# Optimization experiments

Measured on AMD Instinct MI355X. Metric: run time of the kernel, lower is better.

Reference implementation:

```python
import jax, jax.numpy as jnp
import numpy as np

C_S, C_P, C_H, H, P_QK, P_V = 384, 128, 16, 12, 4, 8
B, N = 1, 512
INF = 1e5
EPS = 1e-8


def quat_to_rot(q):
    w, x, y, z = q[..., 0], q[..., 1], q[..., 2], q[..., 3]
    return jnp.stack([
        jnp.stack([1 - 2 * (y * y + z * z), 2 * (x * y - w * z), 2 * (x * z + w * y)], -1),
        jnp.stack([2 * (x * y + w * z), 1 - 2 * (x * x + z * z), 2 * (y * z - w * x)], -1),
        jnp.stack([2 * (x * z - w * y), 2 * (y * z + w * x), 1 - 2 * (x * x + y * y)], -1),
    ], -2)


def layer_norm(x, g, b):
    m = x.mean(-1, keepdims=True)
    v = ((x - m) ** 2).mean(-1, keepdims=True)
    return (x - m) * jax.lax.rsqrt(v + 1e-5) * g + b


def setup_inputs():
    key = jax.random.key(0)
    ks = iter(jax.random.split(key, 64))

    def w(shape, scale=0.02):
        return jax.random.normal(next(ks), shape, dtype=jnp.float32) * scale

    inp = {}
    inp['s'] = jax.random.normal(next(ks), (B, N, C_S), dtype=jnp.float32)
    inp['p'] = jax.random.normal(next(ks), (B, N, N, C_P), dtype=jnp.float32)
    q = jax.random.normal(next(ks), (B, N, 4), dtype=jnp.float32)
    inp['rot'] = quat_to_rot(q / jnp.linalg.norm(q, axis=-1, keepdims=True))
    inp['trans'] = jax.random.normal(next(ks), (B, N, 3), dtype=jnp.float32)
    inp['mask'] = jnp.ones((B, N), dtype=jnp.float32)
    inp['w_q'] = w((C_S, H * C_H)); inp['b_q'] = jnp.zeros((H * C_H,), jnp.float32)
    inp['w_kv'] = w((C_S, 2 * H * C_H)); inp['b_kv'] = jnp.zeros((2 * H * C_H,), jnp.float32)
    inp['w_qp'] = w((C_S, H * P_QK * 3)); inp['b_qp'] = jnp.zeros((H * P_QK * 3,), jnp.float32)
    inp['w_kvp'] = w((C_S, H * (P_QK + P_V) * 3)); inp['b_kvp'] = jnp.zeros((H * (P_QK + P_V) * 3,), jnp.float32)
    inp['w_b'] = w((C_P, H)); inp['b_b'] = jnp.zeros((H,), jnp.float32)
    inp['head_w'] = w((H,), 0.5)
    d_out = H * (C_H + C_P + P_V * 4)  # 2112
    inp['w_o'] = w((d_out, C_S)); inp['b_o'] = jnp.zeros((C_S,), jnp.float32)
    inp['ln1_g'] = jnp.ones((C_S,), jnp.float32); inp['ln1_b'] = jnp.zeros((C_S,), jnp.float32)
    for i in (1, 2, 3):
        inp['tw%d' % i] = w((C_S, C_S)); inp['tb%d' % i] = jnp.zeros((C_S,), jnp.float32)
    inp['ln2_g'] = jnp.ones((C_S,), jnp.float32); inp['ln2_b'] = jnp.zeros((C_S,), jnp.float32)
    inp['bb_w'] = w((C_S, 6)); inp['bb_b'] = jnp.zeros((6,), jnp.float32)
    return inp


def forward(s, p, rot, trans, mask, w_q, b_q, w_kv, b_kv, w_qp, b_qp, w_kvp, b_kvp,
            w_b, b_b, head_w, w_o, b_o, ln1_g, ln1_b,
            tw1, tb1, tw2, tb2, tw3, tb3, ln2_g, ln2_b, bb_w, bb_b):
    # ---- Invariant Point Attention ----
    q = (s @ w_q + b_q).reshape(B, N, H, C_H)
    k, v = jnp.split((s @ w_kv + b_kv).reshape(B, N, H, 2 * C_H), 2, axis=-1)
    qp = (s @ w_qp + b_qp).reshape(B, N, H * P_QK, 3)
    qp = (jnp.einsum('bnij,bnpj->bnpi', rot, qp) + trans[:, :, None, :]).reshape(B, N, H, P_QK, 3)
    kvp = (s @ w_kvp + b_kvp).reshape(B, N, H * (P_QK + P_V), 3)
    kvp = (jnp.einsum('bnij,bnpj->bnpi', rot, kvp) + trans[:, :, None, :]).reshape(B, N, H, P_QK + P_V, 3)
    kp, vp = kvp[..., :P_QK, :], kvp[..., P_QK:, :]
    bias = p @ w_b + b_b  # [B,N,N,H]
    a = jnp.einsum('bihc,bjhc->bhij', q, k) * float(np.sqrt(1.0 / (3 * C_H)))
    a = a + float(np.sqrt(1.0 / 3)) * jnp.transpose(bias, (0, 3, 1, 2))
    d2 = ((qp[:, :, None] - kp[:, None]) ** 2).sum(-1)  # [B,N,N,H,Pqk]
    hw = jax.nn.softplus(head_w) * float(np.sqrt(1.0 / (3 * (P_QK * 9.0 / 2))))
    pt_att = -0.5 * (d2 * hw[:, None]).sum(-1)  # [B,N,N,H]
    sq_mask = (mask[:, :, None] * mask[:, None, :] - 1.0) * INF  # [B,N,N]
    a = jax.nn.softmax(a + jnp.transpose(pt_att, (0, 3, 1, 2)) + sq_mask[:, None], axis=-1)
    o = jnp.einsum('bhij,bjhc->bihc', a, v).reshape(B, N, H * C_H)
    op = jnp.einsum('bhij,bjhpc->bihpc', a, vp) - trans[:, :, None, None, :]
    op = jnp.einsum('bnji,bnhpj->bnhpi', rot, op)  # invert-apply frames
    op_norm = jnp.sqrt((op ** 2).sum(-1) + EPS)  # [B,N,H,Pv]
    o_pair = jnp.einsum('bhij,bijc->bihc', a, p).reshape(B, N, H * C_P)
    cat = jnp.concatenate([o, op.reshape(B, N, H * P_V * 3), op_norm.reshape(B, N, H * P_V), o_pair], -1)
    s = s + cat @ w_o + b_o
    s = layer_norm(s, ln1_g, ln1_b)
    # ---- structure transition (1 layer, residual + LN) ----
    h = jax.nn.relu(s @ tw1 + tb1)
    h = jax.nn.relu(h @ tw2 + tb2)
    s = layer_norm(s + h @ tw3 + tb3, ln2_g, ln2_b)
    # ---- backbone update + frame compose ----
    upd = s @ bb_w + bb_b  # [B,N,6]
    quat = jnp.concatenate([jnp.ones((B, N, 1), s.dtype), upd[..., :3]], -1)
    quat = quat / jnp.linalg.norm(quat, axis=-1, keepdims=True)
    r_u = quat_to_rot(quat)
    rot_new = jnp.einsum('bnij,bnjk->bnik', rot, r_u)
    trans_new = jnp.einsum('bnij,bnj->bni', rot, upd[..., 3:]) + trans
    return s, rot_new, trans_new


def reference(s, p, rot, trans, mask, w_q, b_q, w_kv, b_kv, w_qp, b_qp, w_kvp, b_kvp,
              w_b, b_b, head_w, w_o, b_o, ln1_g, ln1_b,
              tw1, tb1, tw2, tb2, tw3, tb3, ln2_g, ln2_b, bb_w, bb_b):
    return forward(s, p, rot, trans, mask, w_q, b_q, w_kv, b_kv, w_qp, b_qp, w_kvp, b_kvp,
                   w_b, b_b, head_w, w_o, b_o, ln1_g, ln1_b,
                   tw1, tb1, tw2, tb2, tw3, tb3, ln2_g, ln2_b, bb_w, bb_b)
```

## Files before the change

kernel.cpp:

```cpp
#include <hip/hip_runtime.h>
#include <math.h>

#define N 512
#define CS 384
#define CP 128
#define CH 16
#define NH 12
#define NN (N*N)
#define DCAT 2112
#define INFV 100000.0f

__device__ __constant__ float SC_QK = 0.14433756729740643f;
#define SC_B  0.57735026918962576f
#define HW_SC 0.13608276348795434f

typedef __attribute__((ext_vector_type(8))) short bf16x8;
typedef __attribute__((ext_vector_type(4))) float f32x4;
typedef __attribute__((ext_vector_type(4))) short sh4;
typedef __attribute__((ext_vector_type(4))) unsigned u32x4;
typedef unsigned short ushort_t;

__device__ inline short f2bf(float v) {
    unsigned u = __builtin_bit_cast(unsigned, v);
    u += 0x7FFF + ((u >> 16) & 1);
    return (short)(u >> 16);
}
__device__ inline float bf2f(ushort_t u) {
    unsigned x = ((unsigned)u) << 16;
    return __builtin_bit_cast(float, x);
}
__device__ __forceinline__ unsigned cvtpk(float a, float b) {
    unsigned r;
    asm("v_cvt_pk_bf16_f32 %0, %1, %2" : "=v"(r) : "v"(a), "v"(b));
    return r;
}

__device__ __forceinline__ void gload16(const void* g, void* l) {
    __builtin_amdgcn_global_load_lds(
        (const __attribute__((address_space(1))) unsigned int*)g,
        (__attribute__((address_space(3))) unsigned int*)l,
        16, 0, 0);
}

struct FrontArgs {
    const float* wsrc0; const float* wsrc1; const float* wsrc2; const float* wsrc3;
    const float* wsrc4; const float* wsrc5; const float* wsrc6; const float* wsrc7;
    ushort_t* wdst0; ushort_t* wdst1; ushort_t* wdst2; ushort_t* wdst3;
    ushort_t* wdst4; ushort_t* wdst5; ushort_t* wdst6; ushort_t* wdst7;
    const float* s; ushort_t* sbf;
    const float* bq; const float* bkv; const float* bqp; const float* bkvp;
    float* biasp;
    const float* p; const float* w_b; const float* b_b; ushort_t* bias_b;
};

__global__ __launch_bounds__(256) void front_kernel(FrontArgs a)
{
    __shared__ __align__(16) char SM[36864];
    const int b = blockIdx.x;
    const int t = threadIdx.x;
    if (b < 4096) {
        float* Pf = (float*)SM;
        ushort_t* Wbs = (ushort_t*)(SM + 32768);
        const int w = t >> 6;
        const size_t row0 = (size_t)b * 64;

        for (int idx = t; idx < 2048; idx += 256) {
            int h = idx >> 7, c = idx & 127;
            float v = (h < 12) ? a.w_b[c * 12 + h] : 0.f;
            int byte = h * 256 + ((c * 2) ^ ((h & 7) << 4));
            *(ushort_t*)((char*)Wbs + byte) = (ushort_t)f2bf(v);
        }
        #pragma unroll
        for (int k = 0; k < 8; ++k) {
            int s2 = k * 256 + t;
            int row = s2 >> 5, ch = s2 & 31;
            const char* src = (const char*)(a.p + (row0 + row) * 128) + ((ch ^ (row & 7)) * 16);
            gload16(src, (char*)Pf + (size_t)(k * 256 + w * 64) * 16);
        }
        __syncthreads();

        const int l = t & 63, lr = l & 15, hk = l >> 4;
        const int jb = w * 16;
        f32x4 acc = (f32x4){0.f, 0.f, 0.f, 0.f};
        #pragma unroll
        for (int ks = 0; ks < 4; ++ks) {
            int row = jb + lr;
            int kc = ks * 8 + hk * 2;
            const char* base = (const char*)Pf + row * 512;
            f32x4 v0 = *(const f32x4*)(base + ((kc ^ (row & 7)) * 16));
            f32x4 v1 = *(const f32x4*)(base + (((kc + 1) ^ (row & 7)) * 16));
            bf16x8 afr;
            afr[0] = f2bf(v0[0]); afr[1] = f2bf(v0[1]); afr[2] = f2bf(v0[2]); afr[3] = f2bf(v0[3]);
            afr[4] = f2bf(v1[0]); afr[5] = f2bf(v1[1]); afr[6] = f2bf(v1[2]); afr[7] = f2bf(v1[3]);
            bf16x8 bfr = *(const bf16x8*)((char*)Wbs + lr * 256 +
                            ((ks * 64 + hk * 16) ^ ((lr & 7) << 4)));
            acc = __builtin_amdgcn_mfma_f32_16x16x32_bf16(afr, bfr, acc, 0, 0, 0);
        }
        if (lr < 12) {
            float bb = a.b_b[lr];
            size_t gj = row0 + jb + hk * 4;
            sh4 o;
            #pragma unroll
            for (int r = 0; r < 4; ++r) o[r] = f2bf(SC_B * (acc[r] + bb));
            *(sh4*)(a.bias_b + (size_t)lr * NN + gj) = o;
        }
    } else {
        const int bp = b - 4096;
        if (bp < 1668) {
            const float* src; ushort_t* dst; int begin, nx, Nc, K;
            if      (bp < 72)   { src=a.wsrc0; dst=a.wdst0; begin=0;    nx=6;  Nc=192; K=384; }
            else if (bp < 216)  { src=a.wsrc1; dst=a.wdst1; begin=72;   nx=12; Nc=384; K=384; }
            else if (bp < 276)  { src=a.wsrc2; dst=a.wdst2; begin=216;  nx=5;  Nc=144; K=384; }
            else if (bp < 444)  { src=a.wsrc3; dst=a.wdst3; begin=276;  nx=14; Nc=432; K=384; }
            else if (bp < 1236) { src=a.wsrc4; dst=a.wdst4; begin=444;  nx=12; Nc=384; K=2112; }
            else if (bp < 1380) { src=a.wsrc5; dst=a.wdst5; begin=1236; nx=12; Nc=384; K=384; }
            else if (bp < 1524) { src=a.wsrc6; dst=a.wdst6; begin=1380; nx=12; Nc=384; K=384; }
            else                { src=a.wsrc7; dst=a.wdst7; begin=1524; nx=12; Nc=384; K=384; }
            int lb = bp - begin;
            int cx = (lb % nx) * 32, ky = (lb / nx) * 32;
            float (*tile)[33] = (float(*)[33])SM;
            const int tx = t & 31, ty = t >> 5;
            for (int r = ty; r < 32; r += 8) {
                int c = cx + tx;
                tile[r][tx] = (c < Nc) ? src[(size_t)(ky + r) * Nc + c] : 0.f;
            }
            __syncthreads();
            for (int r = ty; r < 32; r += 8) {
                int orow = cx + r;
                if (orow < Nc)
                    dst[(size_t)orow * K + ky + tx] = (ushort_t)f2bf(tile[tx][r]);
            }
        } else if (bp < 1860) {
            int i4 = (bp - 1668) * 256 + t;
            f32x4 v = *(const f32x4*)(a.s + (size_t)i4 * 4);
            sh4 o;
            o[0] = f2bf(v[0]); o[1] = f2bf(v[1]); o[2] = f2bf(v[2]); o[3] = f2bf(v[3]);
            *(sh4*)(a.sbf + (size_t)i4 * 4) = o;
        } else {
            for (int idx = t; idx < 1152; idx += 256) {
                float v;
                if (idx < 192)      v = a.bq[idx];
                else if (idx < 576) v = a.bkv[idx - 192];
                else if (idx < 720) v = a.bqp[idx - 576];
                else                v = a.bkvp[idx - 720];
                a.biasp[idx] = v;
            }
        }
    }
}

__global__ __launch_bounds__(256) void gemm_bf16(
    const ushort_t* __restrict__ A, const ushort_t* __restrict__ Bt,
    float* __restrict__ part, int K, int KOUT, int nk)
{
    __shared__ __align__(16) ushort_t As[2][2048];
    __shared__ __align__(16) ushort_t Bs[2][2048];
    const int t = threadIdx.x, w = t >> 6, l = t & 63;
    const int i0 = blockIdx.x * 64, n0 = blockIdx.y * 64, sp = blockIdx.z;
    const int kbase = sp * nk * 32;

    const int srow = w * 16 + (l >> 2);
    const int skb = (l & 3) ^ ((srow >> 1) & 3);
    const ushort_t* aSrc = A + (size_t)(i0 + srow) * K + kbase + skb * 8;
    const ushort_t* bSrc = Bt + (size_t)(n0 + srow) * K + kbase + skb * 8;
    ushort_t* aDst = &As[0][0] + w * 512;
    ushort_t* bDst = &Bs[0][0] + w * 512;

    const int r0 = (w >> 1) * 32, c0 = (w & 1) * 32, lr = l & 15, hk = l >> 4;
    int aOff[2], bOff[2];
    #pragma unroll
    for (int m = 0; m < 2; ++m) {
        int row = r0 + m * 16 + lr;
        aOff[m] = row * 64 + ((hk ^ ((row >> 1) & 3)) << 4);
    }
    #pragma unroll
    for (int n = 0; n < 2; ++n) {
        int row = c0 + n * 16 + lr;
        bOff[n] = row * 64 + ((hk ^ ((row >> 1) & 3)) << 4);
    }

    f32x4 acc[2][2];
    #pragma unroll
    for (int m = 0; m < 2; ++m)
        #pragma unroll
        for (int n = 0; n < 2; ++n) acc[m][n] = (f32x4){0.f, 0.f, 0.f, 0.f};

    gload16(aSrc, aDst);
    gload16(bSrc, bDst);
    __syncthreads();

    int cur = 0;
    for (int it = 0; it < nk; ++it) {
        if (it + 1 < nk) {
            gload16(aSrc + (it + 1) * 32, aDst + (cur ^ 1) * 2048);
            gload16(bSrc + (it + 1) * 32, bDst + (cur ^ 1) * 2048);
        }
        const char* ab = (const char*)&As[cur][0];
        const char* bb = (const char*)&Bs[cur][0];
        bf16x8 a0 = *(const bf16x8*)(ab + aOff[0]);
        bf16x8 a1 = *(const bf16x8*)(ab + aOff[1]);
        bf16x8 b0 = *(const bf16x8*)(bb + bOff[0]);
        bf16x8 b1 = *(const bf16x8*)(bb + bOff[1]);
        acc[0][0] = __builtin_amdgcn_mfma_f32_16x16x32_bf16(a0, b0, acc[0][0], 0, 0, 0);
        acc[0][1] = __builtin_amdgcn_mfma_f32_16x16x32_bf16(a0, b1, acc[0][1], 0, 0, 0);
        acc[1][0] = __builtin_amdgcn_mfma_f32_16x16x32_bf16(a1, b0, acc[1][0], 0, 0, 0);
        acc[1][1] = __builtin_amdgcn_mfma_f32_16x16x32_bf16(a1, b1, acc[1][1], 0, 0, 0);
        __syncthreads();
        cur ^= 1;
    }

    #pragma unroll
    for (int m = 0; m < 2; ++m)
        #pragma unroll
        for (int n = 0; n < 2; ++n) {
            int col = n0 + c0 + n * 16 + lr;
            int rowb = i0 + r0 + m * 16 + (l >> 4) * 4;
            float* pr = part + ((size_t)sp * 512 + rowb) * KOUT + col;
            #pragma unroll
            for (int j = 0; j < 4; ++j)
                pr[(size_t)j * KOUT] = acc[m][n][j];
        }
}

__global__ __launch_bounds__(256) void gemm_red(
    const float* __restrict__ partsIn, const float* __restrict__ kbias,
    const ushort_t* __restrict__ Bt, float* __restrict__ partOut, int nk)
{
    __shared__ __align__(16) ushort_t As[2][2048];
    __shared__ __align__(16) ushort_t Bs[2][2048];
    const int t = threadIdx.x, w = t >> 6, l = t & 63;
    const int i0 = blockIdx.x * 64, n0 = blockIdx.y * 64, sp = blockIdx.z;
    const int kbase = sp * nk * 32;

    const int srow = w * 16 + (l >> 2);
    const int skb = (l & 3) ^ ((srow >> 1) & 3);
    const ushort_t* bSrc = Bt + (size_t)(n0 + srow) * 384 + kbase + skb * 8;
    ushort_t* bDst = &Bs[0][0] + w * 512;

    const int ar = t >> 2, apch = t & 3;
    const int agch = apch ^ ((ar >> 1) & 3);
    const float* aBase = partsIn + (size_t)(i0 + ar) * 384 + kbase + agch * 8;
    const int aByte = ar * 64 + apch * 16;

    const int r0 = (w >> 1) * 32, c0 = (w & 1) * 32, lr = l & 15, hk = l >> 4;
    int aOff[2], bOff[2];
    #pragma unroll
    for (int m = 0; m < 2; ++m) {
        int row = r0 + m * 16 + lr;
        aOff[m] = row * 64 + ((hk ^ ((row >> 1) & 3)) << 4);
    }
    #pragma unroll
    for (int n = 0; n < 2; ++n) {
        int row = c0 + n * 16 + lr;
        bOff[n] = row * 64 + ((hk ^ ((row >> 1) & 3)) << 4);
    }

    f32x4 av0, av1;
    #define A_LOAD(it)                                                            \
        {                                                                         \
            const float* ap = aBase + (it) * 32;                                  \
            av0 = *(const f32x4*)(ap) + *(const f32x4*)(ap + 196608)              \
                + *(const f32x4*)(ap + 393216);                                   \
            av1 = *(const f32x4*)(ap + 4) + *(const f32x4*)(ap + 196608 + 4)      \
                + *(const f32x4*)(ap + 393216 + 4);                               \
        }
    #define A_STORE(buf, it)                                                      \
        {                                                                         \
            int kk = kbase + (it) * 32 + agch * 8;                                \
            f32x4 kb0 = *(const f32x4*)(kbias + kk);                              \
            f32x4 kb1 = *(const f32x4*)(kbias + kk + 4);                          \
            f32x4 s0 = av0 + kb0, s1 = av1 + kb1;                                 \
            u32x4 pk;                                                             \
            pk[0] = cvtpk(fmaxf(s0[0], 0.f), fmaxf(s0[1], 0.f));                  \
            pk[1] = cvtpk(fmaxf(s0[2], 0.f), fmaxf(s0[3], 0.f));                  \
            pk[2] = cvtpk(fmaxf(s1[0], 0.f), fmaxf(s1[1], 0.f));                  \
            pk[3] = cvtpk(fmaxf(s1[2], 0.f), fmaxf(s1[3], 0.f));                  \
            *(u32x4*)((char*)&As[buf][0] + aByte) = pk;                           \
        }

    f32x4 acc[2][2];
    #pragma unroll
    for (int m = 0; m < 2; ++m)
        #pragma unroll
        for (int n = 0; n < 2; ++n) acc[m][n] = (f32x4){0.f, 0.f, 0.f, 0.f};

    gload16(bSrc, bDst);
    A_LOAD(0);
    A_STORE(0, 0);
    __syncthreads();

    int cur = 0;
    for (int it = 0; it < nk; ++it) {
        if (it + 1 < nk) {
            gload16(bSrc + (it + 1) * 32, bDst + (cur ^ 1) * 2048);
            A_LOAD(it + 1);
        }
        const char* ab = (const char*)&As[cur][0];
        const char* bb = (const char*)&Bs[cur][0];
        bf16x8 a0 = *(const bf16x8*)(ab + aOff[0]);
        bf16x8 a1 = *(const bf16x8*)(ab + aOff[1]);
        bf16x8 b0 = *(const bf16x8*)(bb + bOff[0]);
        bf16x8 b1 = *(const bf16x8*)(bb + bOff[1]);
        acc[0][0] = __builtin_amdgcn_mfma_f32_16x16x32_bf16(a0, b0, acc[0][0], 0, 0, 0);
        acc[0][1] = __builtin_amdgcn_mfma_f32_16x16x32_bf16(a0, b1, acc[0][1], 0, 0, 0);
        acc[1][0] = __builtin_amdgcn_mfma_f32_16x16x32_bf16(a1, b0, acc[1][0], 0, 0, 0);
        acc[1][1] = __builtin_amdgcn_mfma_f32_16x16x32_bf16(a1, b1, acc[1][1], 0, 0, 0);
        if (it + 1 < nk) A_STORE(cur ^ 1, it + 1);
        __syncthreads();
        cur ^= 1;
    }
    #undef A_LOAD
    #undef A_STORE

    #pragma unroll
    for (int m = 0; m < 2; ++m)
        #pragma unroll
        for (int n = 0; n < 2; ++n) {
            int col = n0 + c0 + n * 16 + lr;
            int rowb = i0 + r0 + m * 16 + (l >> 4) * 4;
            float* pr = partOut + ((size_t)sp * 512 + rowb) * 384 + col;
            #pragma unroll
            for (int j = 0; j < 4; ++j)
                pr[(size_t)j * 384] = acc[m][n][j];
        }
}

__global__ void reduce_ln(const float* __restrict__ parts, int S,
                          const float* __restrict__ gbias, const float* __restrict__ resid,
                          const float* __restrict__ g, const float* __restrict__ b,
                          float* __restrict__ outf, ushort_t* __restrict__ outbf,
                          const float* __restrict__ bb_w, const float* __restrict__ bb_b,
                          const float* __restrict__ rot, const float* __restrict__ trans,
                          float* __restrict__ out_rot, float* __restrict__ out_trans)
{
    __shared__ float buf[384];
    __shared__ float red[2], red2[2];
    __shared__ float ush[2][6];
    const int i = blockIdx.x, t = threadIdx.x;
    float s = 0.f, sq = 0.f;
    for (int k = t; k < 384; k += 128) {
        float v = gbias[k] + resid[(size_t)i * 384 + k];
        for (int s2 = 0; s2 < S; ++s2)
            v += parts[((size_t)s2 * 512 + i) * 384 + k];
        buf[k] = v; s += v; sq += v * v;
    }
    for (int off = 32; off; off >>= 1) { s += __shfl_xor(s, off); sq += __shfl_xor(sq, off); }
    if ((t & 63) == 0) { red[t >> 6] = s; red2[t >> 6] = sq; }
    __syncthreads();
    float mean = (red[0] + red[1]) * (1.0f / 384.0f);
    float var = (red2[0] + red2[1]) * (1.0f / 384.0f) - mean * mean;
    float rstd = rsqrtf(var + 1e-5f);
    float onorm[3];
    #pragma unroll
    for (int kk = 0; kk < 3; ++kk) {
        int k = t + kk * 128;
        float o = (buf[k] - mean) * rstd * g[k] + b[k];
        onorm[kk] = o;
        if (outf) outf[(size_t)i * 384 + k] = o;
        if (outbf) outbf[(size_t)i * 384 + k] = (ushort_t)f2bf(o);
    }
    if (!bb_w) return;
    float u[6] = {0.f, 0.f, 0.f, 0.f, 0.f, 0.f};
    #pragma unroll
    for (int kk = 0; kk < 3; ++kk) {
        int k = t + kk * 128;
        float sv = onorm[kk];
        #pragma unroll
        for (int c = 0; c < 6; ++c) u[c] += sv * bb_w[k * 6 + c];
    }
    #pragma unroll
    for (int c = 0; c < 6; ++c)
        for (int off = 32; off; off >>= 1) u[c] += __shfl_xor(u[c], off);
    if ((t & 63) == 0) {
        #pragma unroll
        for (int c = 0; c < 6; ++c) ush[t >> 6][c] = u[c];
    }
    __syncthreads();
    if (t == 0) {
        float uu[6];
        #pragma unroll
        for (int c = 0; c < 6; ++c) uu[c] = ush[0][c] + ush[1][c] + bb_b[c];
        float inq = rsqrtf(1.0f + uu[0]*uu[0] + uu[1]*uu[1] + uu[2]*uu[2]);
        float w = inq, x = uu[0]*inq, y = uu[1]*inq, z = uu[2]*inq;
        float Ru[9];
        Ru[0] = 1.f - 2.f*(y*y + z*z); Ru[1] = 2.f*(x*y - w*z); Ru[2] = 2.f*(x*z + w*y);
        Ru[3] = 2.f*(x*y + w*z); Ru[4] = 1.f - 2.f*(x*x + z*z); Ru[5] = 2.f*(y*z - w*x);
        Ru[6] = 2.f*(x*z - w*y); Ru[7] = 2.f*(y*z + w*x); Ru[8] = 1.f - 2.f*(x*x + y*y);
        const float* R = rot + i * 9;
        #pragma unroll
        for (int a = 0; a < 3; ++a) {
            #pragma unroll
            for (int cc = 0; cc < 3; ++cc)
                out_rot[i * 9 + a * 3 + cc] =
                    R[a*3+0]*Ru[0+cc] + R[a*3+1]*Ru[3+cc] + R[a*3+2]*Ru[6+cc];
            out_trans[i * 3 + a] = R[a*3+0]*uu[3] + R[a*3+1]*uu[4] + R[a*3+2]*uu[5]
                                   + trans[i * 3 + a];
        }
    }
}

__global__ __launch_bounds__(256) void postproj_kernel(
    const float* __restrict__ parts, const float* __restrict__ biasp,
    const float* __restrict__ rot, const float* __restrict__ trans,
    const float* __restrict__ head_w, const float* __restrict__ mask,
    ushort_t* __restrict__ Qext, ushort_t* __restrict__ Kext, ushort_t* __restrict__ Vext)
{
    __shared__ float buf[1152];
    __shared__ float hwv[12], kc28[12];
    const int j = blockIdx.x, t = threadIdx.x;
    for (int c = t; c < 1152; c += 256)
        buf[c] = biasp[c] + parts[(size_t)j * 1152 + c] + parts[(size_t)(512 + j) * 1152 + c];
    if (t >= 192 && t < 204) {
        int h = t - 192;
        hwv[h] = HW_SC * log1pf(expf(head_w[h]));
    }
    __syncthreads();
    if (t < 192) {
        int base = 576 + t * 3;
        const float* R = rot + j * 9;
        const float* T = trans + j * 3;
        float x = buf[base], y = buf[base + 1], z = buf[base + 2];
        float nx = R[0]*x + R[1]*y + R[2]*z + T[0];
        float ny = R[3]*x + R[4]*y + R[5]*z + T[1];
        float nz = R[6]*x + R[7]*y + R[8]*z + T[2];
        buf[base] = nx; buf[base + 1] = ny; buf[base + 2] = nz;
    }
    __syncthreads();
    if (t < 12) {
        float s2 = 0.f;
        #pragma unroll
        for (int e = 0; e < 12; ++e) { float v = buf[720 + t * 36 + e]; s2 += v * v; }
        kc28[t] = -0.5f * hwv[t] * s2 + (mask[j] - 1.0f) * INFV;
    }
    __syncthreads();
    if (t < 192) {
        int h = t >> 4, c0 = (t & 15) * 2;
        float hwf = hwv[h];
        #pragma unroll
        for (int e = 0; e < 2; ++e) {
            int c = c0 + e;
            float qv, kv2;
            if (c < 16)      { qv = SC_QK * buf[h * 16 + c];           kv2 = buf[192 + h * 32 + c]; }
            else if (c < 28) { qv = hwf * buf[576 + h * 12 + (c - 16)]; kv2 = buf[720 + h * 36 + (c - 16)]; }
            else if (c == 28){ qv = 1.f;                               kv2 = kc28[h]; }
            else             { qv = 0.f;                               kv2 = 0.f; }
            Qext[(size_t)h * 16384 + j * 32 + c] = (ushort_t)f2bf(qv);
            Kext[(size_t)h * 16384 + j * 32 + c] = (ushort_t)f2bf(kv2);
        }
    }
    for (int idx = t; idx < 576; idx += 256) {
        int h = idx / 48, c = idx % 48;
        float v;
        if (c < 16)      v = buf[192 + h * 32 + 16 + c];
        else if (c < 40) v = buf[720 + h * 36 + 12 + (c - 16)];
        else             v = 0.f;
        Vext[(size_t)h * 24576 + c * 512 + j] = (ushort_t)f2bf(v);
    }
}

__global__ __launch_bounds__(256) void attn_mfma(
    const ushort_t* __restrict__ Qext, const ushort_t* __restrict__ Kext,
    const ushort_t* __restrict__ bias_b, const ushort_t* __restrict__ Vext,
    const float* __restrict__ rot, const float* __restrict__ trans,
    ushort_t* __restrict__ attn_b, ushort_t* __restrict__ catb)
{
    __shared__ float sc[16 * 516];
    __shared__ float redm[64];
    __shared__ float invr[16];
    __shared__ float opl[16][25];
    const int t = threadIdx.x, w = t >> 6, l = t & 63;
    const int i0 = blockIdx.x * 16, h = blockIdx.y;
    const int lr = l & 15, hk = l >> 4;

    #pragma unroll
    for (int it = 0; it < 8; ++it) {
        int elem = (t + it * 256) * 4;
        int i = elem >> 9, j = elem & 511;
        sh4 raw = *(const sh4*)(bias_b + (size_t)h * NN + (size_t)(i0 + i) * 512 + j);
        f32x4 v;
        v[0] = bf2f((ushort_t)raw[0]); v[1] = bf2f((ushort_t)raw[1]);
        v[2] = bf2f((ushort_t)raw[2]); v[3] = bf2f((ushort_t)raw[3]);
        *(f32x4*)(sc + i * 516 + j) = v;
    }
    __syncthreads();

    bf16x8 a0 = *(const bf16x8*)(Qext + (size_t)h * 16384 + (i0 + lr) * 32 + hk * 8);
    f32x4 acc[8];
    #pragma unroll
    for (int n = 0; n < 8; ++n) {
        bf16x8 b = *(const bf16x8*)(Kext + (size_t)h * 16384 +
                                    (w * 128 + n * 16 + lr) * 32 + hk * 8);
        acc[n] = __builtin_amdgcn_mfma_f32_16x16x32_bf16(a0, b, (f32x4){0.f,0.f,0.f,0.f}, 0, 0, 0);
    }

    float rmax[4] = {-3.0e38f, -3.0e38f, -3.0e38f, -3.0e38f};
    #pragma unroll
    for (int n = 0; n < 8; ++n) {
        int col = w * 128 + n * 16 + lr;
        #pragma unroll
        for (int r = 0; r < 4; ++r) {
            int row = hk * 4 + r;
            float v = acc[n][r] + sc[row * 516 + col];
            sc[row * 516 + col] = v;
            rmax[r] = fmaxf(rmax[r], v);
        }
    }
    #pragma unroll
    for (int r = 0; r < 4; ++r) {
        float v = rmax[r];
        v = fmaxf(v, __shfl_xor(v, 1));
        v = fmaxf(v, __shfl_xor(v, 2));
        v = fmaxf(v, __shfl_xor(v, 4));
        v = fmaxf(v, __shfl_xor(v, 8));
        if (lr == 0) redm[w * 16 + hk * 4 + r] = v;
    }
    __syncthreads();

    {
        int row = t >> 4, g = t & 15;
        float mx = fmaxf(fmaxf(redm[row], redm[16 + row]),
                         fmaxf(redm[32 + row], redm[48 + row]));
        float sum = 0.f;
        float* sr = sc + row * 516;
        for (int c = g; c < 512; c += 16) {
            float e = expf(sr[c] - mx);
            sr[c] = e;
            sum += e;
        }
        sum += __shfl_xor(sum, 1);
        sum += __shfl_xor(sum, 2);
        sum += __shfl_xor(sum, 4);
        sum += __shfl_xor(sum, 8);
        if (g == 0) invr[row] = 1.0f / sum;
    }
    __syncthreads();

    #pragma unroll
    for (int it = 0; it < 8; ++it) {
        int elem = (t + it * 256) * 4;
        int i = elem >> 9, j = elem & 511;
        f32x4 v = *(const f32x4*)(sc + i * 516 + j);
        float iv = invr[i];
        sh4 o;
        o[0] = f2bf(v[0] * iv); o[1] = f2bf(v[1] * iv);
        o[2] = f2bf(v[2] * iv); o[3] = f2bf(v[3] * iv);
        *(sh4*)(attn_b + (size_t)h * NN + (size_t)(i0 + i) * 512 + j) = o;
    }

    f32x4 acc3[3];
    acc3[0] = (f32x4){0.f,0.f,0.f,0.f};
    acc3[1] = (f32x4){0.f,0.f,0.f,0.f};
    acc3[2] = (f32x4){0.f,0.f,0.f,0.f};
    const ushort_t* vbase = Vext + (size_t)h * 24576 + lr * 512 + hk * 8;
    #pragma unroll
    for (int kt = 0; kt < 16; ++kt) {
        const float* srow = sc + lr * 516 + kt * 32 + hk * 8;
        f32x4 x0 = *(const f32x4*)(srow);
        f32x4 x1 = *(const f32x4*)(srow + 4);
        u32x4 ap;
        ap[0] = cvtpk(x0[0], x0[1]); ap[1] = cvtpk(x0[2], x0[3]);
        ap[2] = cvtpk(x1[0], x1[1]); ap[3] = cvtpk(x1[2], x1[3]);
        bf16x8 af = __builtin_bit_cast(bf16x8, ap);
        #pragma unroll
        for (int n = 0; n < 3; ++n) {
            bf16x8 bf = *(const bf16x8*)(vbase + n * 16 * 512 + kt * 32);
            acc3[n] = __builtin_amdgcn_mfma_f32_16x16x32_bf16(af, bf, acc3[n], 0, 0, 0);
        }
    }
    #pragma unroll
    for (int n = 0; n < 3; ++n) {
        int c = n * 16 + lr;
        #pragma unroll
        for (int r = 0; r < 4; ++r) {
            int ri = hk * 4 + r;
            float val = acc3[n][r] * invr[ri];
            if (c < 16)
                catb[(size_t)(i0 + ri) * DCAT + h * 16 + c] = (ushort_t)f2bf(val);
            else if (c < 40)
                opl[ri][c - 16] = val;
        }
    }
    __syncthreads();
    if (t < 128) {
        int i16 = t >> 3, pv = t & 7;
        int i = i0 + i16;
        const float* T = trans + i * 3;
        const float* R = rot + i * 9;
        float x = opl[i16][pv * 3 + 0] - T[0];
        float y = opl[i16][pv * 3 + 1] - T[1];
        float z = opl[i16][pv * 3 + 2] - T[2];
        float rx = R[0] * x + R[3] * y + R[6] * z;
        float ry = R[1] * x + R[4] * y + R[7] * z;
        float rz = R[2] * x + R[5] * y + R[8] * z;
        float nm = sqrtf(rx * rx + ry * ry + rz * rz + 1e-8f);
        ushort_t* cr = catb + (size_t)i * DCAT;
        cr[192 + h * 24 + pv * 3 + 0] = (ushort_t)f2bf(rx);
        cr[192 + h * 24 + pv * 3 + 1] = (ushort_t)f2bf(ry);
        cr[192 + h * 24 + pv * 3 + 2] = (ushort_t)f2bf(rz);
        cr[480 + h * 8 + pv] = (ushort_t)f2bf(nm);
    }
}

__global__ __launch_bounds__(256) void opair_mfma(
    const ushort_t* __restrict__ attn_b, const float* __restrict__ p,
    ushort_t* __restrict__ catb)
{
    __shared__ __align__(16) ushort_t As2[16 * 512];
    __shared__ __align__(16) ushort_t Pt[2][128 * 72];
    const int t = threadIdx.x, i = blockIdx.x;
    const int w = t >> 6, l = t & 63;
    const int lr = l & 15, hk = l >> 4;

    #pragma unroll
    for (int ii = 0; ii < 4; ++ii) {
        int idx = (t + ii * 256) * 8;
        int h = idx >> 9, j = idx & 511;
        bf16x8 v;
        if (h < 12) v = *(const bf16x8*)(attn_b + (size_t)h * NN + (size_t)i * 512 + j);
        else        v = (bf16x8){0,0,0,0,0,0,0,0};
        *(bf16x8*)((char*)As2 + h * 1024 + ((j * 2) ^ ((h & 7) << 4))) = v;
    }

    const int jA = (t >> 3) * 2;
    const int c0 = (t & 7) * 16;
    const float* psrc = p + (size_t)i * 65536;

    f32x4 va[4], vb[4];
    #pragma unroll
    for (int q = 0; q < 4; ++q) {
        va[q] = *(const f32x4*)(psrc + (size_t)jA * 128 + c0 + q * 4);
        vb[q] = *(const f32x4*)(psrc + (size_t)(jA + 1) * 128 + c0 + q * 4);
    }

    #define PACK_TILE(buf)                                                       \
        {                                                                        \
            ushort_t* ptw = &Pt[buf][0];                                         \
            _Pragma("unroll")                                                    \
            for (int e = 0; e < 16; ++e) {                                       \
                int c = c0 + e;                                                  \
                unsigned pk = cvtpk(va[e >> 2][e & 3], vb[e >> 2][e & 3]);       \
                int byte = c * 144 + ((jA * 2) ^ (((c >> 4) & 7) << 4));         \
                *(unsigned*)((char*)ptw + byte) = pk;                            \
            }                                                                    \
        }
    #define LOAD_TILE(tile)                                                      \
        {                                                                        \
            const float* s0 = psrc + (size_t)((tile) * 64 + jA) * 128 + c0;      \
            _Pragma("unroll")                                                    \
            for (int q = 0; q < 4; ++q) {                                        \
                va[q] = *(const f32x4*)(s0 + q * 4);                             \
                vb[q] = *(const f32x4*)(s0 + 128 + q * 4);                       \
            }                                                                    \
        }

    PACK_TILE(0);
    LOAD_TILE(1);

    f32x4 acc[2];
    acc[0] = (f32x4){0.f, 0.f, 0.f, 0.f};
    acc[1] = (f32x4){0.f, 0.f, 0.f, 0.f};

    int cur = 0;
    for (int tile = 0; tile < 8; ++tile) {
        __syncthreads();
        const char* pt = (const char*)&Pt[cur][0];
        #pragma unroll
        for (int ks = 0; ks < 2; ++ks) {
            bf16x8 afr = *(const bf16x8*)((char*)As2 + lr * 1024 +
                            ((tile * 128 + ks * 64 + hk * 16) ^ ((lr & 7) << 4)));
            #pragma unroll
            for (int n = 0; n < 2; ++n) {
                int c = w * 32 + n * 16 + lr;
                bf16x8 bfr = *(const bf16x8*)(pt + c * 144 +
                                ((ks * 64 + hk * 16) ^ (((c >> 4) & 7) << 4)));
                acc[n] = __builtin_amdgcn_mfma_f32_16x16x32_bf16(afr, bfr, acc[n], 0, 0, 0);
            }
        }
        if (tile < 7) {
            PACK_TILE(cur ^ 1);
            if (tile < 6) LOAD_TILE(tile + 2);
            cur ^= 1;
        }
    }
    #undef PACK_TILE
    #undef LOAD_TILE
    #pragma unroll
    for (int n = 0; n < 2; ++n) {
        int c = w * 32 + n * 16 + lr;
        #pragma unroll
        for (int r = 0; r < 4; ++r) {
            int h = hk * 4 + r;
            if (h < 12)
                catb[(size_t)i * DCAT + 576 + h * 128 + c] = (ushort_t)f2bf(acc[n][r]);
        }
    }
}

extern "C" void kernel_launch(void* const* d_in, const int* in_sizes, int n_in,
                              void* d_out, int out_size, void* d_ws, size_t ws_size,
                              hipStream_t stream)
{
    const float* s      = (const float*)d_in[0];
    const float* p      = (const float*)d_in[1];
    const float* rot    = (const float*)d_in[2];
    const float* trans  = (const float*)d_in[3];
    const float* mask   = (const float*)d_in[4];
    const float* w_q    = (const float*)d_in[5];
    const float* b_q    = (const float*)d_in[6];
    const float* w_kv   = (const float*)d_in[7];
    const float* b_kv   = (const float*)d_in[8];
    const float* w_qp   = (const float*)d_in[9];
    const float* b_qp   = (const float*)d_in[10];
    const float* w_kvp  = (const float*)d_in[11];
    const float* b_kvp  = (const float*)d_in[12];
    const float* w_b    = (const float*)d_in[13];
    const float* b_b    = (const float*)d_in[14];
    const float* head_w = (const float*)d_in[15];
    const float* w_o    = (const float*)d_in[16];
    const float* b_o    = (const float*)d_in[17];
    const float* ln1_g  = (const float*)d_in[18];
    const float* ln1_b  = (const float*)d_in[19];
    const float* tw1    = (const float*)d_in[20];
    const float* tb1    = (const float*)d_in[21];
    const float* tw2    = (const float*)d_in[22];
    const float* tb2    = (const float*)d_in[23];
    const float* tw3    = (const float*)d_in[24];
    const float* tb3    = (const float*)d_in[25];
    const float* ln2_g  = (const float*)d_in[26];
    const float* ln2_b  = (const float*)d_in[27];
    const float* bb_w   = (const float*)d_in[28];
    const float* bb_b   = (const float*)d_in[29];

    float* ws = (float*)d_ws;
    float*    parts  = ws;
    float*    partsB = parts + 589824;
    float*    s1     = parts + 1179648;
    float*    biasp  = s1 + 196608;
    ushort_t* ub     = (ushort_t*)(biasp + 1152);
    ushort_t* bias_b = ub;
    ushort_t* attn_b = bias_b + 3145728;
    ushort_t* catb   = attn_b + 3145728;
    ushort_t* sbf    = catb + 1081344;
    ushort_t* s1bf   = sbf + 196608;
    ushort_t* h1bf   = s1bf + 196608;
    ushort_t* h2bf   = h1bf + 196608;
    ushort_t* Qext   = h2bf + 196608;
    ushort_t* Kext   = Qext + 196608;
    ushort_t* Vext   = Kext + 196608;
    ushort_t* Wtp    = Vext + 294912;
    ushort_t* Wto    = Wtp + 442368;
    ushort_t* Wt1    = Wto + 811008;
    ushort_t* Wt2    = Wt1 + 147456;
    ushort_t* Wt3    = Wt2 + 147456;

    float* out_s     = (float*)d_out;
    float* out_rot   = out_s + 196608;
    float* out_trans = out_rot + 4608;

    FrontArgs fa;
    fa.wsrc0 = w_q;  fa.wdst0 = Wtp;
    fa.wsrc1 = w_kv; fa.wdst1 = Wtp + (size_t)192 * 384;
    fa.wsrc2 = w_qp; fa.wdst2 = Wtp + (size_t)576 * 384;
    fa.wsrc3 = w_kvp; fa.wdst3 = Wtp + (size_t)720 * 384;
    fa.wsrc4 = w_o;  fa.wdst4 = Wto;
    fa.wsrc5 = tw1;  fa.wdst5 = Wt1;
    fa.wsrc6 = tw2;  fa.wdst6 = Wt2;
    fa.wsrc7 = tw3;  fa.wdst7 = Wt3;
    fa.s = s; fa.sbf = sbf;
    fa.bq = b_q; fa.bkv = b_kv; fa.bqp = b_qp; fa.bkvp = b_kvp;
    fa.biasp = biasp;
    fa.p = p; fa.w_b = w_b; fa.b_b = b_b; fa.bias_b = bias_b;
    front_kernel<<<5957, 256, 0, stream>>>(fa);

    gemm_bf16<<<dim3(8, 18, 2), 256, 0, stream>>>(sbf, Wtp, parts, 384, 1152, 6);
    postproj_kernel<<<512, 256, 0, stream>>>(parts, biasp, rot, trans, head_w, mask,
                                             Qext, Kext, Vext);

    attn_mfma<<<dim3(32, 12), 256, 0, stream>>>(Qext, Kext, bias_b, Vext, rot, trans,
                                                attn_b, catb);
    opair_mfma<<<512, 256, 0, stream>>>(attn_b, p, catb);

    gemm_bf16<<<dim3(8, 6, 6), 256, 0, stream>>>(catb, Wto, parts, 2112, 384, 11);
    reduce_ln<<<512, 128, 0, stream>>>(parts, 6, b_o, s, ln1_g, ln1_b, s1, s1bf,
                                       nullptr, nullptr, nullptr, nullptr, nullptr, nullptr);

    gemm_bf16<<<dim3(8, 6, 3), 256, 0, stream>>>(s1bf, Wt1, parts, 384, 384, 4);
    gemm_red<<<dim3(8, 6, 3), 256, 0, stream>>>(parts, tb1, Wt2, partsB, 4);
    gemm_red<<<dim3(8, 6, 3), 256, 0, stream>>>(partsB, tb2, Wt3, parts, 4);
    reduce_ln<<<512, 128, 0, stream>>>(parts, 3, tb3, s1, ln2_g, ln2_b, out_s, nullptr,
                                       bb_w, bb_b, rot, trans, out_rot, out_trans);
}
```

Before: 124.7 us.

## Split opair reduction over j across two 256-thread groups per block

The o_pair kernel now runs 512 threads per block, and each half of the block handles 256 of the 512 j positions, using smaller 32-row p tiles with their own double-buffered LDS staging. The two partial accumulators are combined through an LDS scratch buffer before the bf16 store. The aim is more memory-level parallelism when streaming the 256 KB p slice per row, so each block finishes its load phase sooner. The cost is more LDS, an extra barrier, and a cross-group reduction, which may lower occupancy.

```diff
diff --git a/kernel.cpp b/kernel.cpp
--- a/kernel.cpp
+++ b/kernel.cpp
@@ -601,19 +601,22 @@
     }
 }
 
-__global__ __launch_bounds__(256) void opair_mfma(
+__global__ __launch_bounds__(512) void opair_mfma(
     const ushort_t* __restrict__ attn_b, const float* __restrict__ p,
     ushort_t* __restrict__ catb)
 {
     __shared__ __align__(16) ushort_t As2[16 * 512];
-    __shared__ __align__(16) ushort_t Pt[2][128 * 72];
+    __shared__ __align__(16) ushort_t Pt[2][2][128 * 40];
+    __shared__ float scr[2048];
     const int t = threadIdx.x, i = blockIdx.x;
-    const int w = t >> 6, l = t & 63;
+    const int g = t >> 8, tl = t & 255;
+    const int w = tl >> 6, l = t & 63;
     const int lr = l & 15, hk = l >> 4;
-
-    #pragma unroll
-    for (int ii = 0; ii < 4; ++ii) {
-        int idx = (t + ii * 256) * 8;
+    const int jbase = g * 256;
+
+    #pragma unroll
+    for (int ii = 0; ii < 2; ++ii) {
+        int idx = (t + ii * 512) * 8;
         int h = idx >> 9, j = idx & 511;
         bf16x8 v;
         if (h < 12) v = *(const bf16x8*)(attn_b + (size_t)h * NN + (size_t)i * 512 + j);
@@ -621,38 +624,32 @@
         *(bf16x8*)((char*)As2 + h * 1024 + ((j * 2) ^ ((h & 7) << 4))) = v;
     }
 
-    const int jA = (t >> 3) * 2;
-    const int c0 = (t & 7) * 16;
-    const float* psrc = p + (size_t)i * 65536;
-
-    f32x4 va[4], vb[4];
-    #pragma unroll
-    for (int q = 0; q < 4; ++q) {
-        va[q] = *(const f32x4*)(psrc + (size_t)jA * 128 + c0 + q * 4);
-        vb[q] = *(const f32x4*)(psrc + (size_t)(jA + 1) * 128 + c0 + q * 4);
-    }
-
+    const int jp = tl >> 4, jl = jp * 2;
+    const int cg = tl & 15, c0 = cg * 8;
+    const float* psrc = p + (size_t)i * 65536 + (size_t)jbase * 128;
+
+    f32x4 va[2], vb[2];
+    #define LOAD_TILE(tile)                                                      \
+        {                                                                        \
+            const float* s0 = psrc + (size_t)((tile) * 32 + jl) * 128 + c0;      \
+            va[0] = *(const f32x4*)(s0);                                         \
+            va[1] = *(const f32x4*)(s0 + 4);                                     \
+            vb[0] = *(const f32x4*)(s0 + 128);                                   \
+            vb[1] = *(const f32x4*)(s0 + 132);                                   \
+        }
     #define PACK_TILE(buf)                                                       \
         {                                                                        \
-            ushort_t* ptw = &Pt[buf][0];                                         \
+            ushort_t* ptw = &Pt[g][buf][0];                                      \
             _Pragma("unroll")                                                    \
-            for (int e = 0; e < 16; ++e) {                                       \
+            for (int e = 0; e < 8; ++e) {                                        \
                 int c = c0 + e;                                                  \
                 unsigned pk = cvtpk(va[e >> 2][e & 3], vb[e >> 2][e & 3]);       \
-                int byte = c * 144 + ((jA * 2) ^ (((c >> 4) & 7) << 4));         \
+                int byte = c * 80 + ((jl * 2) ^ (((c >> 2) & 3) << 4));          \
                 *(unsigned*)((char*)ptw + byte) = pk;                            \
             }                                                                    \
         }
-    #define LOAD_TILE(tile)                                                      \
-        {                                                                        \
-            const float* s0 = psrc + (size_t)((tile) * 64 + jA) * 128 + c0;      \
-            _Pragma("unroll")                                                    \
-            for (int q = 0; q < 4; ++q) {                                        \
-                va[q] = *(const f32x4*)(s0 + q * 4);                             \
-                vb[q] = *(const f32x4*)(s0 + 128 + q * 4);                       \
-            }                                                                    \
-        }
-
+
+    LOAD_TILE(0);
     PACK_TILE(0);
     LOAD_TILE(1);
 
@@ -663,18 +660,15 @@
     int cur = 0;
     for (int tile = 0; tile < 8; ++tile) {
         __syncthreads();
-        const char* pt = (const char*)&Pt[cur][0];
-        #pragma unroll
-        for (int ks = 0; ks < 2; ++ks) {
-            bf16x8 afr = *(const bf16x8*)((char*)As2 + lr * 1024 +
-                            ((tile * 128 + ks * 64 + hk * 16) ^ ((lr & 7) << 4)));
-            #pragma unroll
-            for (int n = 0; n < 2; ++n) {
-                int c = w * 32 + n * 16 + lr;
-                bf16x8 bfr = *(const bf16x8*)(pt + c * 144 +
-                                ((ks * 64 + hk * 16) ^ (((c >> 4) & 7) << 4)));
-                acc[n] = __builtin_amdgcn_mfma_f32_16x16x32_bf16(afr, bfr, acc[n], 0, 0, 0);
-            }
+        const char* pt = (const char*)&Pt[g][cur][0];
+        bf16x8 afr = *(const bf16x8*)((char*)As2 + lr * 1024 +
+                        ((jbase * 2 + tile * 64 + hk * 16) ^ ((lr & 7) << 4)));
+        #pragma unroll
+        for (int n = 0; n < 2; ++n) {
+            int c = w * 32 + n * 16 + lr;
+            bf16x8 bfr = *(const bf16x8*)(pt + c * 80 +
+                            ((hk * 16) ^ (((c >> 2) & 3) << 4)));
+            acc[n] = __builtin_amdgcn_mfma_f32_16x16x32_bf16(afr, bfr, acc[n], 0, 0, 0);
         }
         if (tile < 7) {
             PACK_TILE(cur ^ 1);
@@ -684,14 +678,26 @@
     }
     #undef PACK_TILE
     #undef LOAD_TILE
-    #pragma unroll
-    for (int n = 0; n < 2; ++n) {
-        int c = w * 32 + n * 16 + lr;
-        #pragma unroll
-        for (int r = 0; r < 4; ++r) {
-            int h = hk * 4 + r;
-            if (h < 12)
-                catb[(size_t)i * DCAT + 576 + h * 128 + c] = (ushort_t)f2bf(acc[n][r]);
+
+    if (g == 1) {
+        #pragma unroll
+        for (int n = 0; n < 2; ++n)
+            #pragma unroll
+            for (int r = 0; r < 4; ++r)
+                scr[((w * 64 + l) * 2 + n) * 4 + r] = acc[n][r];
+    }
+    __syncthreads();
+    if (g == 0) {
+        #pragma unroll
+        for (int n = 0; n < 2; ++n) {
+            int c = w * 32 + n * 16 + lr;
+            #pragma unroll
+            for (int r = 0; r < 4; ++r) {
+                int h = hk * 4 + r;
+                float v = acc[n][r] + scr[((w * 64 + l) * 2 + n) * 4 + r];
+                if (h < 12)
+                    catb[(size_t)i * DCAT + 576 + h * 128 + c] = (ushort_t)f2bf(v);
+            }
         }
     }
 }
@@ -778,7 +784,7 @@
 
     attn_mfma<<<dim3(32, 12), 256, 0, stream>>>(Qext, Kext, bias_b, Vext, rot, trans,
                                                 attn_b, catb);
-    opair_mfma<<<512, 256, 0, stream>>>(attn_b, p, catb);
+    opair_mfma<<<512, 512, 0, stream>>>(attn_b, p, catb);
 
     gemm_bf16<<<dim3(8, 6, 6), 256, 0, stream>>>(catb, Wto, parts, 2112, 384, 11);
     reduce_ln<<<512, 128, 0, stream>>>(parts, 6, b_o, s, ln1_g, ln1_b, s1, s1bf,
```

Result: no change. 126.3 us (+1.3%).
